# Kernel optimization log

Measured on AMD Instinct MI355X. Metric: run time of the kernel, lower is better.

## Reference

```python
import jax, jax.numpy as jnp
import numpy as np

B, C, N = 8, 256, 2048
H = max(1, C // 8)  # hidden = in_channels // 8 = 32


def setup_inputs() -> dict:
    key = jax.random.key(0)
    ks = jax.random.split(key, 7)
    s = 0.05
    return {
        "x": jax.random.normal(ks[0], (B, C, N), dtype=jnp.float32),
        "wq": jax.random.normal(ks[1], (H, C), dtype=jnp.float32) * s,
        "bq": jax.random.normal(ks[2], (H,), dtype=jnp.float32) * s,
        "wk": jax.random.normal(ks[3], (H, C), dtype=jnp.float32) * s,
        "bk": jax.random.normal(ks[4], (H,), dtype=jnp.float32) * s,
        "wv": jax.random.normal(ks[5], (C, C), dtype=jnp.float32) * s,
        "bv": jax.random.normal(ks[6], (C,), dtype=jnp.float32) * s,
    }


def reference(x, wq, bq, wk, bk, wv, bv):
    # 1x1 Conv1d == per-position linear: weight [out, in]
    q = jnp.einsum('bcn,hc->bnh', x, wq) + bq                  # [B, N, H] (already permuted)
    k = jnp.einsum('bcn,hc->bhn', x, wk) + bk[None, :, None]   # [B, H, N]
    v = jnp.einsum('bcn,dc->bdn', x, wv) + bv[None, :, None]   # [B, C, N]
    energy = jnp.einsum('bnh,bhm->bnm', q, k)                  # [B, N, N] (no scaling, as in source)
    weights = jax.nn.softmax(energy, axis=-1)                  # softmax over last dim
    # out = bmm(value, weights^T): out[b,c,i] = sum_j v[b,c,j] * weights[b,i,j]
    out = jnp.einsum('bcj,bij->bci', v, weights)               # [B, C, N]
    return out + x
```

## Files before the change

### kernel.cpp

```cpp
#include <hip/hip_runtime.h>
#include <hip/hip_bf16.h>
#include <cstdint>
#include <cstddef>

#define B_ 8
#define C_ 256
#define N_ 2048
#define H_ 32
#define VP_ 2064
#define NT_ (N_ / 64)

typedef __bf16 bf8 __attribute__((ext_vector_type(8)));
typedef __bf16 bf4 __attribute__((ext_vector_type(4)));
typedef float f4 __attribute__((ext_vector_type(4)));
typedef float f16v __attribute__((ext_vector_type(16)));

__device__ inline void gload_lds16(const void* g, void* l) {
  __builtin_amdgcn_global_load_lds(
      (const __attribute__((address_space(1))) unsigned int*)g,
      (__attribute__((address_space(3))) unsigned int*)l, 16, 0, 0);
}

__global__ __launch_bounds__(256) void pack_kernel(
    const float* __restrict__ wq, const float* __restrict__ wk,
    const float* __restrict__ wv, const float* __restrict__ bq,
    const float* __restrict__ bk, const float* __restrict__ bv,
    __hip_bfloat16* __restrict__ wpk, float* __restrict__ bpk) {
  const float L2E = 1.44269504088896f;
  int r = blockIdx.x, c = threadIdx.x;
  float v;
  if (r < 256)      v = wv[r * 256 + c];
  else if (r < 288) v = wq[(r - 256) * 256 + c] * L2E;
  else              v = wk[(r - 288) * 256 + c];
  wpk[r * 256 + c] = __float2bfloat16(v);
  if (c == 0) bpk[r] = (r < 256) ? bv[r] : (r < 288 ? bq[r - 256] * L2E : bk[r - 288]);
}

__global__ __launch_bounds__(256) void proj_kernel(
    const float* __restrict__ x, const __hip_bfloat16* __restrict__ wpk,
    const float* __restrict__ bpk, __hip_bfloat16* __restrict__ vbf,
    __hip_bfloat16* __restrict__ qkb) {
  __shared__ __attribute__((aligned(16))) __hip_bfloat16 As[2][320 * 32];
  int tid = threadIdx.x, wv = tid >> 6, lane = tid & 63;
  int b = blockIdx.y;
  int n0 = blockIdx.x * 32;
  int fcol = lane & 15, hi4 = lane >> 4;
  int grow = lane >> 2, gc = (lane & 3) * 8;
  const float* xb = x + (size_t)b * C_ * N_;

#pragma unroll
  for (int g = 0; g < 5; ++g)
    gload_lds16(wpk + (size_t)(wv * 80 + g * 16 + grow) * 256 + gc,
                &As[0][(wv * 80 + g * 16) * 32]);
  float xr[2][8];
#pragma unroll
  for (int j = 0; j < 2; ++j)
#pragma unroll
    for (int e = 0; e < 8; ++e)
      xr[j][e] = xb[(size_t)(hi4 * 8 + e) * N_ + n0 + j * 16 + fcol];

  f4 acc[5][2] = {};
  for (int t = 0; t < 8; ++t) {
    int buf = t & 1;
    __syncthreads();
    if (t < 7) {
      int k1 = (t + 1) * 32;
#pragma unroll
      for (int g = 0; g < 5; ++g)
        gload_lds16(wpk + (size_t)(wv * 80 + g * 16 + grow) * 256 + k1 + gc,
                    &As[buf ^ 1][(wv * 80 + g * 16) * 32]);
    }
    bf8 bfr[2];
#pragma unroll
    for (int j = 0; j < 2; ++j)
#pragma unroll
      for (int e = 0; e < 8; ++e) bfr[j][e] = (__bf16)xr[j][e];
    if (t < 7) {
      int k1 = (t + 1) * 32;
#pragma unroll
      for (int j = 0; j < 2; ++j)
#pragma unroll
        for (int e = 0; e < 8; ++e)
          xr[j][e] = xb[(size_t)(k1 + hi4 * 8 + e) * N_ + n0 + j * 16 + fcol];
    }
#pragma unroll
    for (int s = 0; s < 5; ++s) {
      bf8 af = *(const bf8*)&As[buf][(wv * 80 + s * 16 + fcol) * 32 + hi4 * 8];
      acc[s][0] = __builtin_amdgcn_mfma_f32_16x16x32_bf16(af, bfr[0], acc[s][0], 0, 0, 0);
      acc[s][1] = __builtin_amdgcn_mfma_f32_16x16x32_bf16(af, bfr[1], acc[s][1], 0, 0, 0);
    }
  }
  int rq = hi4 * 4;
#pragma unroll
  for (int s = 0; s < 5; ++s)
#pragma unroll
    for (int r = 0; r < 4; ++r) {
      int m = wv * 80 + s * 16 + rq + r;
      float bias = bpk[m];
#pragma unroll
      for (int j = 0; j < 2; ++j) {
        int n = n0 + j * 16 + fcol;
        float val = acc[s][j][r] + bias;
        if (m < 256)
          vbf[((size_t)b * C_ + m) * VP_ + n] = __float2bfloat16(val);
        else
          qkb[((size_t)b * N_ + n) * 64 + (m - 256)] = __float2bfloat16(val);
      }
    }
}

#define ATTN_BODY(T, BUF, CK0, CK1, CV0, CV1, CV2, CV3,                        \
                  NK0, NK1, NV0, NV1, NV2, NV3)                                \
  {                                                                            \
    int tn_ = (T) + 1 < NT_ ? (T) + 1 : (T);                                   \
    const __hip_bfloat16* kpn_ = kp + (size_t)tn_ * 64 * 64;                   \
    NK0 = *(const bf8*)kpn_;                                                   \
    NK1 = *(const bf8*)(kpn_ + 16);                                            \
    const __hip_bfloat16* vpn_ = vR + tn_ * 64;                                \
    NV0 = *(const bf8*)vpn_;                                                   \
    NV1 = *(const bf8*)(vpn_ + 16);                                            \
    NV2 = *(const bf8*)(vpn_ + 32);                                            \
    NV3 = *(const bf8*)(vpn_ + 48);                                            \
    f16v s = {};                                                               \
    s = __builtin_amdgcn_mfma_f32_32x32x16_bf16(CK0, qf0, s, 0, 0, 0);         \
    s = __builtin_amdgcn_mfma_f32_32x32x16_bf16(CK1, qf1, s, 0, 0, 0);         \
    _Pragma("unroll")                                                          \
    for (int r = 0; r < 16; ++r) s[r] = __builtin_amdgcn_exp2f(s[r]);          \
    _Pragma("unroll")                                                          \
    for (int r = 0; r < 16; r += 2) { lp0 += s[r]; lp1 += s[r + 1]; }          \
    __hip_bfloat16* pw_ = &pS[BUF][iw * 32 + l31][jw * 32 + 4 * hi];           \
    _Pragma("unroll")                                                          \
    for (int q = 0; q < 4; ++q) {                                              \
      bf4 tb_;                                                                 \
      tb_[0] = (__bf16)s[4 * q + 0];                                           \
      tb_[1] = (__bf16)s[4 * q + 1];                                           \
      tb_[2] = (__bf16)s[4 * q + 2];                                           \
      tb_[3] = (__bf16)s[4 * q + 3];                                           \
      *(bf4*)(pw_ + 8 * q) = tb_;                                              \
    }                                                                          \
    asm volatile("s_waitcnt lgkmcnt(0)" ::: "memory");                         \
    __builtin_amdgcn_s_barrier();                                              \
    const __hip_bfloat16* pr_ = &pS[BUF][iw * 32 + l31][hi * 8];               \
    __builtin_amdgcn_s_setprio(1);                                             \
    {                                                                          \
      bf8 pf0_ = *(const bf8*)(pr_ + 0);                                       \
      acc = __builtin_amdgcn_mfma_f32_32x32x16_bf16(CV0, pf0_, acc, 0, 0, 0);  \
      bf8 pf1_ = *(const bf8*)(pr_ + 16);                                      \
      acc = __builtin_amdgcn_mfma_f32_32x32x16_bf16(CV1, pf1_, acc, 0, 0, 0);  \
      bf8 pf2_ = *(const bf8*)(pr_ + 32);                                      \
      acc = __builtin_amdgcn_mfma_f32_32x32x16_bf16(CV2, pf2_, acc, 0, 0, 0);  \
      bf8 pf3_ = *(const bf8*)(pr_ + 48);                                      \
      acc = __builtin_amdgcn_mfma_f32_32x32x16_bf16(CV3, pf3_, acc, 0, 0, 0);  \
    }                                                                          \
    __builtin_amdgcn_s_setprio(0);                                             \
  }

__global__ __launch_bounds__(256, 4) void fused_attn(
    const __hip_bfloat16* __restrict__ qk,
    const __hip_bfloat16* __restrict__ vbf,
    const float* __restrict__ x, float* __restrict__ out) {
  __shared__ __attribute__((aligned(16))) __hip_bfloat16 pS[2][64][88];
  __shared__ float lSp[2][64];
  int tid = threadIdx.x;
  int w = tid >> 6, lane = tid & 63;
  int l31 = lane & 31, hi = lane >> 5;
  int jw = w & 1, iw = w >> 1;
  int blk = blockIdx.x;
  int b = blk & 7;
  int rest = blk >> 3;
  int cs = rest & 3;
  int i0 = (rest >> 2) * 64;

  const __hip_bfloat16* qkB = qk + (size_t)b * N_ * 64;
  const __hip_bfloat16* qp = qkB + (size_t)(i0 + iw * 32 + l31) * 64 + hi * 8;
  bf8 qf0 = *(const bf8*)qp;
  bf8 qf1 = *(const bf8*)(qp + 16);
  const __hip_bfloat16* kp = qkB + (size_t)(jw * 32 + l31) * 64 + 32 + hi * 8;
  const __hip_bfloat16* vR =
      vbf + ((size_t)b * C_ + cs * 64 + jw * 32 + l31) * VP_ + hi * 8;

  bf8 kA0 = *(const bf8*)kp;
  bf8 kA1 = *(const bf8*)(kp + 16);
  bf8 vA0 = *(const bf8*)vR;
  bf8 vA1 = *(const bf8*)(vR + 16);
  bf8 vA2 = *(const bf8*)(vR + 32);
  bf8 vA3 = *(const bf8*)(vR + 48);
  bf8 kB0, kB1, vB0, vB1, vB2, vB3;

  f16v acc = {};
  float lp0 = 0.f, lp1 = 0.f;

  for (int tt = 0; tt < NT_; tt += 2) {
    ATTN_BODY(tt, 0, kA0, kA1, vA0, vA1, vA2, vA3,
              kB0, kB1, vB0, vB1, vB2, vB3)
    ATTN_BODY(tt + 1, 1, kB0, kB1, vB0, vB1, vB2, vB3,
              kA0, kA1, vA0, vA1, vA2, vA3)
  }

  float lp = lp0 + lp1;
  lp += __shfl_xor(lp, 32);
  if (lane < 32) lSp[jw][iw * 32 + l31] = lp;
  __syncthreads();
  float linv = 1.0f / (lSp[0][iw * 32 + l31] + lSp[1][iw * 32 + l31]);

  const float* xr = x + (size_t)b * C_ * N_;
  float* op = out + (size_t)b * C_ * N_;
  int i = i0 + iw * 32 + l31;
#pragma unroll
  for (int r = 0; r < 16; ++r) {
    int crow = (r & 3) + 8 * (r >> 2) + 4 * hi;
    size_t o = (size_t)(cs * 64 + jw * 32 + crow) * N_ + i;
    op[o] = acc[r] * linv + xr[o];
  }
}

extern "C" void kernel_launch(void* const* d_in, const int* in_sizes, int n_in,
                              void* d_out, int out_size, void* d_ws, size_t ws_size,
                              hipStream_t stream) {
  const float* x  = (const float*)d_in[0];
  const float* wq = (const float*)d_in[1];
  const float* bq = (const float*)d_in[2];
  const float* wk = (const float*)d_in[3];
  const float* bk = (const float*)d_in[4];
  const float* wv = (const float*)d_in[5];
  const float* bv = (const float*)d_in[6];
  float* out = (float*)d_out;

  char* ws = (char*)d_ws;
  __hip_bfloat16* qkb = (__hip_bfloat16*)ws;
  __hip_bfloat16* vbf = (__hip_bfloat16*)(ws + (2u << 20));
  __hip_bfloat16* wpk = (__hip_bfloat16*)(ws + 10551296u);
  float*          bpk = (float*)(ws + 10551296u + 163840u);

  pack_kernel<<<dim3(320), 256, 0, stream>>>(wq, wk, wv, bq, bk, bv, wpk, bpk);
  proj_kernel<<<dim3(N_ / 32, B_), 256, 0, stream>>>(x, wpk, bpk, vbf, qkb);
  fused_attn<<<dim3(1024), 256, 0, stream>>>(qkb, vbf, x, out);
}
```

Measured before the change: 151.7 us.

## Keep softmax probabilities in registers and split key range across waves

The attention kernel is restructured so each wave computes 16x16 score tiles for all 64 queries over its own key slice. The exponentiated probabilities feed the PV MFMAs directly from registers, which removes the per-tile LDS round trip and barrier. The V layout written by the projection kernel is swizzled so the register layout of P matches the V operand. Each block now covers 128 channels instead of 64, halving the grid and recomputing QK^T less often. Partial accumulators from the two key halves are reduced through LDS at the end and written with vectorized coalesced stores, at the cost of more registers and lower occupancy (launch bounds 2).

```diff
diff --git a/kernel.cpp b/kernel.cpp
--- a/kernel.cpp
+++ b/kernel.cpp
@@ -13,7 +13,6 @@
 typedef __bf16 bf8 __attribute__((ext_vector_type(8)));
 typedef __bf16 bf4 __attribute__((ext_vector_type(4)));
 typedef float f4 __attribute__((ext_vector_type(4)));
-typedef float f16v __attribute__((ext_vector_type(16)));
 
 __device__ inline void gload_lds16(const void* g, void* l) {
   __builtin_amdgcn_global_load_lds(
@@ -101,116 +100,141 @@
       for (int j = 0; j < 2; ++j) {
         int n = n0 + j * 16 + fcol;
         float val = acc[s][j][r] + bias;
-        if (m < 256)
-          vbf[((size_t)b * C_ + m) * VP_ + n] = __float2bfloat16(val);
-        else
+        if (m < 256) {
+          int nsw = n0 + ((fcol >> 2) << 3) + (j << 2) + (fcol & 3);
+          vbf[((size_t)b * C_ + m) * VP_ + nsw] = __float2bfloat16(val);
+        } else {
           qkb[((size_t)b * N_ + n) * 64 + (m - 256)] = __float2bfloat16(val);
+        }
       }
     }
 }
 
-#define ATTN_BODY(T, BUF, CK0, CK1, CV0, CV1, CV2, CV3,                        \
-                  NK0, NK1, NV0, NV1, NV2, NV3)                                \
+#define ATTN_BODY(T, KS)                                                       \
   {                                                                            \
-    int tn_ = (T) + 1 < NT_ ? (T) + 1 : (T);                                   \
-    const __hip_bfloat16* kpn_ = kp + (size_t)tn_ * 64 * 64;                   \
-    NK0 = *(const bf8*)kpn_;                                                   \
-    NK1 = *(const bf8*)(kpn_ + 16);                                            \
-    const __hip_bfloat16* vpn_ = vR + tn_ * 64;                                \
-    NV0 = *(const bf8*)vpn_;                                                   \
-    NV1 = *(const bf8*)(vpn_ + 16);                                            \
-    NV2 = *(const bf8*)(vpn_ + 32);                                            \
-    NV3 = *(const bf8*)(vpn_ + 48);                                            \
-    f16v s = {};                                                               \
-    s = __builtin_amdgcn_mfma_f32_32x32x16_bf16(CK0, qf0, s, 0, 0, 0);         \
-    s = __builtin_amdgcn_mfma_f32_32x32x16_bf16(CK1, qf1, s, 0, 0, 0);         \
+    f4 s0[4], s1[4];                                                           \
     _Pragma("unroll")                                                          \
-    for (int r = 0; r < 16; ++r) s[r] = __builtin_amdgcn_exp2f(s[r]);          \
+    for (int is = 0; is < 4; ++is) {                                           \
+      f4 z = {};                                                               \
+      s0[is] = __builtin_amdgcn_mfma_f32_16x16x32_bf16(KS[0], qf[is], z, 0, 0, 0); \
+      s1[is] = __builtin_amdgcn_mfma_f32_16x16x32_bf16(KS[1], qf[is], z, 0, 0, 0); \
+    }                                                                          \
+    {                                                                          \
+      int tn_ = (T) + 2 < NT_ ? (T) + 2 : NT_ - 1;                             \
+      KS[0] = *(const bf8*)(kp + (size_t)(tn_ * 64) * 64);                     \
+      KS[1] = *(const bf8*)(kp + (size_t)(tn_ * 64 + 16) * 64);                \
+    }                                                                          \
+    bf8 pa[4];                                                                 \
     _Pragma("unroll")                                                          \
-    for (int r = 0; r < 16; r += 2) { lp0 += s[r]; lp1 += s[r + 1]; }          \
-    __hip_bfloat16* pw_ = &pS[BUF][iw * 32 + l31][jw * 32 + 4 * hi];           \
+    for (int is = 0; is < 4; ++is) {                                           \
+      _Pragma("unroll")                                                        \
+      for (int m = 0; m < 4; ++m) {                                            \
+        s0[is][m] = __builtin_amdgcn_exp2f(s0[is][m]);                         \
+        s1[is][m] = __builtin_amdgcn_exp2f(s1[is][m]);                         \
+      }                                                                        \
+      lp[is] += s0[is][0] + s0[is][1] + s0[is][2] + s0[is][3]                  \
+              + s1[is][0] + s1[is][1] + s1[is][2] + s1[is][3];                 \
+      _Pragma("unroll")                                                        \
+      for (int m = 0; m < 4; ++m) {                                            \
+        pa[is][m]     = (__bf16)s0[is][m];                                     \
+        pa[is][4 + m] = (__bf16)s1[is][m];                                     \
+      }                                                                        \
+    }                                                                          \
+    __builtin_amdgcn_s_setprio(1);                                             \
     _Pragma("unroll")                                                          \
-    for (int q = 0; q < 4; ++q) {                                              \
-      bf4 tb_;                                                                 \
-      tb_[0] = (__bf16)s[4 * q + 0];                                           \
-      tb_[1] = (__bf16)s[4 * q + 1];                                           \
-      tb_[2] = (__bf16)s[4 * q + 2];                                           \
-      tb_[3] = (__bf16)s[4 * q + 3];                                           \
-      *(bf4*)(pw_ + 8 * q) = tb_;                                              \
-    }                                                                          \
-    asm volatile("s_waitcnt lgkmcnt(0)" ::: "memory");                         \
-    __builtin_amdgcn_s_barrier();                                              \
-    const __hip_bfloat16* pr_ = &pS[BUF][iw * 32 + l31][hi * 8];               \
-    __builtin_amdgcn_s_setprio(1);                                             \
+    for (int cs = 0; cs < 4; ++cs)                                             \
+      _Pragma("unroll")                                                        \
+      for (int is = 0; is < 4; ++is)                                           \
+        acc[cs][is] = __builtin_amdgcn_mfma_f32_16x16x32_bf16(                 \
+            pa[is], vb[cs], acc[cs][is], 0, 0, 0);                             \
+    __builtin_amdgcn_s_setprio(0);                                             \
     {                                                                          \
-      bf8 pf0_ = *(const bf8*)(pr_ + 0);                                       \
-      acc = __builtin_amdgcn_mfma_f32_32x32x16_bf16(CV0, pf0_, acc, 0, 0, 0);  \
-      bf8 pf1_ = *(const bf8*)(pr_ + 16);                                      \
-      acc = __builtin_amdgcn_mfma_f32_32x32x16_bf16(CV1, pf1_, acc, 0, 0, 0);  \
-      bf8 pf2_ = *(const bf8*)(pr_ + 32);                                      \
-      acc = __builtin_amdgcn_mfma_f32_32x32x16_bf16(CV2, pf2_, acc, 0, 0, 0);  \
-      bf8 pf3_ = *(const bf8*)(pr_ + 48);                                      \
-      acc = __builtin_amdgcn_mfma_f32_32x32x16_bf16(CV3, pf3_, acc, 0, 0, 0);  \
-    }                                                                          \
-    __builtin_amdgcn_s_setprio(0);                                             \
-  }
-
-__global__ __launch_bounds__(256, 4) void fused_attn(
+      int tn_ = (T) + 1 < NT_ ? (T) + 1 : NT_ - 1;                             \
+      _Pragma("unroll")                                                        \
+      for (int cs = 0; cs < 4; ++cs)                                           \
+        vb[cs] = *(const bf8*)(vBp + (size_t)cs * 16 * VP_ + tn_ * 64);        \
+    }                                                                          \
+  }
+
+__global__ __launch_bounds__(256, 2) void fused_attn(
     const __hip_bfloat16* __restrict__ qk,
     const __hip_bfloat16* __restrict__ vbf,
     const float* __restrict__ x, float* __restrict__ out) {
-  __shared__ __attribute__((aligned(16))) __hip_bfloat16 pS[2][64][88];
+  __shared__ __attribute__((aligned(16))) float aS[2][128][68];
   __shared__ float lSp[2][64];
+  __shared__ __attribute__((aligned(16))) float linvS[64];
   int tid = threadIdx.x;
-  int w = tid >> 6, lane = tid & 63;
-  int l31 = lane & 31, hi = lane >> 5;
-  int jw = w & 1, iw = w >> 1;
+  int wv = tid >> 6, lane = tid & 63;
+  int li = lane & 15, lg = lane >> 4;
+  int lg8 = lg * 8, lg4 = lg * 4;
+  int cw = wv >> 1, jw = wv & 1;
   int blk = blockIdx.x;
   int b = blk & 7;
   int rest = blk >> 3;
-  int cs = rest & 3;
-  int i0 = (rest >> 2) * 64;
+  int c0 = (rest & 1) * 128;
+  int i0 = (rest >> 1) * 64;
 
   const __hip_bfloat16* qkB = qk + (size_t)b * N_ * 64;
-  const __hip_bfloat16* qp = qkB + (size_t)(i0 + iw * 32 + l31) * 64 + hi * 8;
-  bf8 qf0 = *(const bf8*)qp;
-  bf8 qf1 = *(const bf8*)(qp + 16);
-  const __hip_bfloat16* kp = qkB + (size_t)(jw * 32 + l31) * 64 + 32 + hi * 8;
-  const __hip_bfloat16* vR =
-      vbf + ((size_t)b * C_ + cs * 64 + jw * 32 + l31) * VP_ + hi * 8;
-
-  bf8 kA0 = *(const bf8*)kp;
-  bf8 kA1 = *(const bf8*)(kp + 16);
-  bf8 vA0 = *(const bf8*)vR;
-  bf8 vA1 = *(const bf8*)(vR + 16);
-  bf8 vA2 = *(const bf8*)(vR + 32);
-  bf8 vA3 = *(const bf8*)(vR + 48);
-  bf8 kB0, kB1, vB0, vB1, vB2, vB3;
-
-  f16v acc = {};
-  float lp0 = 0.f, lp1 = 0.f;
+  bf8 qf[4];
+#pragma unroll
+  for (int is = 0; is < 4; ++is)
+    qf[is] = *(const bf8*)&qkB[(size_t)(i0 + is * 16 + li) * 64 + lg8];
+  const __hip_bfloat16* kp = qkB + (size_t)(jw * 32 + li) * 64 + 32 + lg8;
+  const __hip_bfloat16* vBp =
+      vbf + ((size_t)b * C_ + c0 + cw * 64 + li) * VP_ + jw * 32 + lg8;
+
+  bf8 kE[2], kO[2], vb[4];
+#pragma unroll
+  for (int js = 0; js < 2; ++js) {
+    kE[js] = *(const bf8*)(kp + (size_t)(js * 16) * 64);
+    kO[js] = *(const bf8*)(kp + (size_t)(64 + js * 16) * 64);
+  }
+#pragma unroll
+  for (int cs = 0; cs < 4; ++cs)
+    vb[cs] = *(const bf8*)(vBp + (size_t)cs * 16 * VP_);
+
+  f4 acc[4][4] = {};
+  float lp[4] = {0.f, 0.f, 0.f, 0.f};
 
   for (int tt = 0; tt < NT_; tt += 2) {
-    ATTN_BODY(tt, 0, kA0, kA1, vA0, vA1, vA2, vA3,
-              kB0, kB1, vB0, vB1, vB2, vB3)
-    ATTN_BODY(tt + 1, 1, kB0, kB1, vB0, vB1, vB2, vB3,
-              kA0, kA1, vA0, vA1, vA2, vA3)
-  }
-
-  float lp = lp0 + lp1;
-  lp += __shfl_xor(lp, 32);
-  if (lane < 32) lSp[jw][iw * 32 + l31] = lp;
+    ATTN_BODY(tt, kE)
+    ATTN_BODY(tt + 1, kO)
+  }
+#undef ATTN_BODY
+
+#pragma unroll
+  for (int cs = 0; cs < 4; ++cs)
+#pragma unroll
+    for (int is = 0; is < 4; ++is)
+      *(f4*)&aS[jw][cw * 64 + cs * 16 + li][is * 16 + lg4] = acc[cs][is];
+
+#pragma unroll
+  for (int is = 0; is < 4; ++is) {
+    lp[is] += __shfl_xor(lp[is], 16);
+    lp[is] += __shfl_xor(lp[is], 32);
+  }
+  if (cw == 0 && lane < 16) {
+#pragma unroll
+    for (int is = 0; is < 4; ++is) lSp[jw][is * 16 + lane] = lp[is];
+  }
   __syncthreads();
-  float linv = 1.0f / (lSp[0][iw * 32 + l31] + lSp[1][iw * 32 + l31]);
-
-  const float* xr = x + (size_t)b * C_ * N_;
-  float* op = out + (size_t)b * C_ * N_;
-  int i = i0 + iw * 32 + l31;
-#pragma unroll
-  for (int r = 0; r < 16; ++r) {
-    int crow = (r & 3) + 8 * (r >> 2) + 4 * hi;
-    size_t o = (size_t)(cs * 64 + jw * 32 + crow) * N_ + i;
-    op[o] = acc[r] * linv + xr[o];
+  if (tid < 64) linvS[tid] = 1.0f / (lSp[0][tid] + lSp[1][tid]);
+  __syncthreads();
+
+  const float* xB = x + ((size_t)b * C_ + c0) * N_ + i0;
+  float* oB = out + ((size_t)b * C_ + c0) * N_ + i0;
+  int cr = tid >> 4, i4 = (tid & 15) * 4;
+  f4 lv = *(const f4*)&linvS[i4];
+#pragma unroll
+  for (int q = 0; q < 8; ++q) {
+    int c = q * 16 + cr;
+    f4 a0 = *(const f4*)&aS[0][c][i4];
+    f4 a1 = *(const f4*)&aS[1][c][i4];
+    f4 xv = *(const f4*)(xB + (size_t)c * N_ + i4);
+    f4 o;
+#pragma unroll
+    for (int e = 0; e < 4; ++e) o[e] = (a0[e] + a1[e]) * lv[e] + xv[e];
+    *(f4*)(oB + (size_t)c * N_ + i4) = o;
   }
 }
 
@@ -234,5 +258,5 @@
 
   pack_kernel<<<dim3(320), 256, 0, stream>>>(wq, wk, wv, bq, bk, bv, wpk, bpk);
   proj_kernel<<<dim3(N_ / 32, B_), 256, 0, stream>>>(x, wpk, bpk, vbf, qkb);
-  fused_attn<<<dim3(1024), 256, 0, stream>>>(qkb, vbf, x, out);
-}
+  fused_attn<<<dim3(512), 256, 0, stream>>>(qkb, vbf, x, out);
+}
```

Result: faster. 131.0 us (-13.7%).
